# Optimization experiments

Hardware: AMD Instinct MI355X
Metric: run time of the kernel (lower is better)

The kernel has to match this reference:

```python
import jax, jax.numpy as jnp
import numpy as np

N_NODES = 100000
N_EDGES = 800000
D_IN = 128
D_H = 512


def _glorot(key, shape):
    fan_in, fan_out = shape[1], shape[0]
    lim = jnp.sqrt(6.0 / (fan_in + fan_out))
    return jax.random.uniform(key, shape, jnp.float32, -lim, lim)


def setup_inputs() -> dict:
    key = jax.random.key(0)
    ks = jax.random.split(key, 16)
    x = jax.random.normal(ks[0], (N_NODES, D_IN), jnp.float32)
    edge_index = jax.random.randint(ks[1], (2, N_EDGES), 0, N_NODES, jnp.int64)
    return {
        "x": x,
        "edge_index": edge_index,
        # SAGEConv layer1: lin_l (neighbors, with bias), lin_r (root, no bias)
        "Wl1": _glorot(ks[2], (D_H, D_IN)), "bl1": jnp.zeros((D_H,), jnp.float32),
        "Wr1": _glorot(ks[3], (D_H, D_IN)),
        # SAGEConv layer2
        "Wl2": _glorot(ks[4], (D_H, D_H)), "bl2": jnp.zeros((D_H,), jnp.float32),
        "Wr2": _glorot(ks[5], (D_H, D_H)),
        # SAGEConv layer3
        "Wl3": _glorot(ks[6], (D_H, D_H)), "bl3": jnp.zeros((D_H,), jnp.float32),
        "Wr3": _glorot(ks[7], (D_H, D_H)),
        # residual projections W, W2 (nn.Linear with bias)
        "Ww": _glorot(ks[8], (D_H, D_IN)), "bw": jnp.zeros((D_H,), jnp.float32),
        "Ww2": _glorot(ks[9], (D_H, D_IN)), "bw2": jnp.zeros((D_H,), jnp.float32),
        # shared PReLU parameter (nn.PReLU default: single param init 0.25)
        "a": jnp.array(0.25, jnp.float32),
    }


def _prelu(x, a):
    return jnp.where(x > 0, x, a * x)


def _sage_conv(x, src, dst, Wl, bl, Wr):
    # mean-aggregate neighbor features x[src] onto dst, then linear + root term
    msg = jax.ops.segment_sum(x[src], dst, num_segments=N_NODES)  # [N, d]
    deg = jax.ops.segment_sum(jnp.ones((src.shape[0],), x.dtype), dst,
                              num_segments=N_NODES)
    agg = msg / jnp.maximum(deg, 1.0)[:, None]
    return agg @ Wl.T + bl + x @ Wr.T


def reference(x, edge_index, Wl1, bl1, Wr1, Wl2, bl2, Wr2, Wl3, bl3, Wr3,
              Ww, bw, Ww2, bw2, a):
    src, dst = edge_index[0], edge_index[1]
    h1 = _prelu(_sage_conv(x, src, dst, Wl1, bl1, Wr1), a)
    h2 = _prelu(_sage_conv(h1 + (x @ Ww.T + bw), src, dst, Wl2, bl2, Wr2), a)
    h3 = _prelu(_sage_conv(h2 + h1 + (x @ Ww2.T + bw2), src, dst, Wl3, bl3, Wr3), a)
    return h3
```

## Files before the change

### kernel.cpp

```cpp
#include <hip/hip_runtime.h>
#include <stddef.h>

#define NN 100000
#define NE 800000
#define DIN 128
#define DH 512
#define MT 782
#define NWG1 (MT * 4)
#define CPX1 (NWG1 / 8)

typedef __attribute__((ext_vector_type(8))) short sh8;
typedef __attribute__((ext_vector_type(4))) float f32x4;

__device__ __forceinline__ unsigned short f2b(float f) {
  unsigned u = __float_as_uint(f);
  return (unsigned short)((u + 0x7FFFu + ((u >> 16) & 1u)) >> 16);
}
__device__ __forceinline__ float b2f(unsigned short s) {
  return __uint_as_float(((unsigned)s) << 16);
}

__device__ __forceinline__ void gload16(const unsigned short* g, unsigned short* l) {
  __builtin_amdgcn_global_load_lds(
      (const __attribute__((address_space(1))) void*)g,
      (__attribute__((address_space(3))) void*)l, 16, 0, 0);
}

#define SCHED_FENCE() __builtin_amdgcn_sched_barrier(0)
#define MEM_FENCE() asm volatile("" ::: "memory")
#define VMCNT(n) asm volatile("s_waitcnt vmcnt(" #n ")" ::: "memory")
#define LGKM0() asm volatile("s_waitcnt lgkmcnt(0)" ::: "memory")


__global__ void k_count(const int* __restrict__ dst, int* __restrict__ cnt) {
  int i = blockIdx.x * blockDim.x + threadIdx.x;
  if (i < NE) atomicAdd(&cnt[dst[i]], 1);
}

__global__ void k_invdeg(const int* __restrict__ cnt, float* __restrict__ inv_deg) {
  int i = blockIdx.x * blockDim.x + threadIdx.x;
  if (i < NN) inv_deg[i] = 1.0f / (float)(cnt[i] > 1 ? cnt[i] : 1);
}

__global__ void k_scan1(const int* __restrict__ cnt, int* __restrict__ excl,
                        int* __restrict__ partials) {
  __shared__ int sh[256];
  int tid = threadIdx.x;
  int base = blockIdx.x * 1024 + tid * 4;
  int v[4]; int s = 0;
#pragma unroll
  for (int i = 0; i < 4; i++) { int idx = base + i; v[i] = (idx < NN) ? cnt[idx] : 0; s += v[i]; }
  sh[tid] = s; __syncthreads();
  for (int off = 1; off < 256; off <<= 1) {
    int t = (tid >= off) ? sh[tid - off] : 0;
    __syncthreads();
    sh[tid] += t;
    __syncthreads();
  }
  int run = sh[tid] - s;
#pragma unroll
  for (int i = 0; i < 4; i++) { int idx = base + i; if (idx < NN) excl[idx] = run; run += v[i]; }
  if (tid == 255) partials[blockIdx.x] = sh[255];
}

__global__ void k_scan2(int* __restrict__ partials, int* __restrict__ row_start, int nparts) {
  __shared__ int sh[128];
  int tid = threadIdx.x;
  int v = (tid < nparts) ? partials[tid] : 0;
  sh[tid] = v; __syncthreads();
  for (int off = 1; off < 128; off <<= 1) {
    int t = (tid >= off) ? sh[tid - off] : 0;
    __syncthreads();
    sh[tid] += t;
    __syncthreads();
  }
  if (tid < nparts) partials[tid] = sh[tid] - v;
  if (tid == 127) row_start[NN] = sh[127];
}

__global__ void k_scan3(int* __restrict__ excl, const int* __restrict__ partials) {
  int i = blockIdx.x * blockDim.x + threadIdx.x;
  if (i < NN) excl[i] += partials[i >> 10];
}

__global__ void k_fill(const int* __restrict__ src, const int* __restrict__ dst,
                       const int* __restrict__ row_start, int* __restrict__ cursor,
                       int* __restrict__ ssrc) {
  int i = blockIdx.x * blockDim.x + threadIdx.x;
  if (i < NE) {
    int d = dst[i];
    int pos = atomicAdd(&cursor[d], 1);
    ssrc[row_start[d] + pos] = src[i];
  }
}


__global__ void k_f2b(const float* __restrict__ src, unsigned short* __restrict__ dst, int n) {
  int i = (blockIdx.x * blockDim.x + threadIdx.x) * 4;
  if (i < n) {
    float4 v = *(const float4*)(src + i);
    ushort4 o;
    o.x = f2b(v.x); o.y = f2b(v.y); o.z = f2b(v.z); o.w = f2b(v.w);
    *(ushort4*)(dst + i) = o;
  }
}


__global__ __launch_bounds__(256) void k_aggb512(
    const unsigned short* __restrict__ z, const int* __restrict__ rs,
    const int* __restrict__ ssrc, const float* __restrict__ inv_deg,
    unsigned short* __restrict__ agg) {
  int w = (blockIdx.x * blockDim.x + threadIdx.x) >> 6;
  int lane = threadIdx.x & 63;
  if (w >= NN) return;
  int e0 = rs[w], e1 = rs[w + 1];
  float acc[8] = {0, 0, 0, 0, 0, 0, 0, 0};
  int e = e0;
  for (; e + 1 < e1; e += 2) {
    int sa = ssrc[e], sb = ssrc[e + 1];
    sh8 va = *(const sh8*)(z + (size_t)sa * DH + lane * 8);
    sh8 vb = *(const sh8*)(z + (size_t)sb * DH + lane * 8);
#pragma unroll
    for (int j = 0; j < 8; ++j) acc[j] += b2f((unsigned short)va[j]) + b2f((unsigned short)vb[j]);
  }
  if (e < e1) {
    int sa = ssrc[e];
    sh8 va = *(const sh8*)(z + (size_t)sa * DH + lane * 8);
#pragma unroll
    for (int j = 0; j < 8; ++j) acc[j] += b2f((unsigned short)va[j]);
  }
  float s0 = inv_deg[w];
  sh8 o;
#pragma unroll
  for (int j = 0; j < 8; ++j) o[j] = (short)f2b(acc[j] * s0);
  *(sh8*)(agg + (size_t)w * DH + lane * 8) = o;
}

__global__ __launch_bounds__(256) void k_aggb128(
    const unsigned short* __restrict__ z, const int* __restrict__ rs,
    const int* __restrict__ ssrc, const float* __restrict__ inv_deg,
    unsigned short* __restrict__ agg) {
  int w = (blockIdx.x * blockDim.x + threadIdx.x) >> 6;
  int lane = threadIdx.x & 63;
  if (w >= NN) return;
  int e0 = rs[w], e1 = rs[w + 1];
  float a0 = 0.f, a1 = 0.f;
  int e = e0;
  for (; e + 1 < e1; e += 2) {
    int sa = ssrc[e], sb = ssrc[e + 1];
    unsigned va = *(const unsigned*)(z + (size_t)sa * DIN + lane * 2);
    unsigned vb = *(const unsigned*)(z + (size_t)sb * DIN + lane * 2);
    a0 += b2f((unsigned short)(va & 0xFFFFu)) + b2f((unsigned short)(vb & 0xFFFFu));
    a1 += b2f((unsigned short)(va >> 16)) + b2f((unsigned short)(vb >> 16));
  }
  if (e < e1) {
    unsigned va = *(const unsigned*)(z + (size_t)ssrc[e] * DIN + lane * 2);
    a0 += b2f((unsigned short)(va & 0xFFFFu));
    a1 += b2f((unsigned short)(va >> 16));
  }
  float s0 = inv_deg[w];
  unsigned o = (unsigned)f2b(a0 * s0) | ((unsigned)f2b(a1 * s0) << 16);
  *(unsigned*)(agg + (size_t)w * DIN + lane * 2) = o;
}


__device__ __forceinline__ void stage_tile(
    unsigned short* ldsA, unsigned short* ldsB,
    const unsigned short* __restrict__ A, int sA, int m0,
    const unsigned short* __restrict__ B, int sB, int n0,
    int k0, int tid) {
  const int w = tid >> 6, l = tid & 63;
  const int kc = (l & 3) * 8;
  const int rsub = l >> 2;
#pragma unroll
  for (int i = 0; i < 2; ++i) {
    int rl = w * 32 + i * 16 + rsub;
    int ra = m0 + rl; if (ra >= NN) ra = NN - 1;
    gload16(A + (size_t)ra * sA + k0 + kc, ldsA + (size_t)(w * 32 + i * 16) * 32);
    gload16(B + (size_t)(n0 + rl) * sB + k0 + kc, ldsB + (size_t)(w * 32 + i * 16) * 32);
  }
}

__device__ __forceinline__ void mfma_step(
    const unsigned short* As, const unsigned short* Bs,
    int wr, int wc, int r16, int kg, f32x4 (&acc)[4][4]) {
  sh8 af[4], bf[4];
#pragma unroll
  for (int i = 0; i < 4; ++i)
    af[i] = *(const sh8*)&As[(wr + i * 16 + r16) * 32 + kg * 8];
#pragma unroll
  for (int j = 0; j < 4; ++j)
    bf[j] = *(const sh8*)&Bs[(wc + j * 16 + r16) * 32 + kg * 8];
#pragma unroll
  for (int i = 0; i < 4; ++i)
#pragma unroll
    for (int j = 0; j < 4; ++j)
      acc[i][j] = __builtin_amdgcn_mfma_f32_16x16x32_bf16(af[i], bf[j], acc[i][j], 0, 0, 0);
}

#define PIPE_WAIT(s, S)                 \
  do {                                  \
    if ((s) < (S) - 2) VMCNT(8);        \
    else if ((s) == (S) - 2) VMCNT(4);  \
    else VMCNT(0);                      \
    SCHED_FENCE();                      \
    __builtin_amdgcn_s_barrier();       \
    MEM_FENCE(); SCHED_FENCE();         \
  } while (0)

#define PIPE_END()                      \
  do {                                  \
    SCHED_FENCE();                      \
    __builtin_amdgcn_s_barrier();       \
    MEM_FENCE(); SCHED_FENCE();         \
  } while (0)

__global__ __launch_bounds__(256, 2) void k_gemm1(
    const unsigned short* __restrict__ ag, const unsigned short* __restrict__ xb,
    const unsigned short* __restrict__ Wl1, const unsigned short* __restrict__ Wr1,
    const unsigned short* __restrict__ Ww, const unsigned short* __restrict__ Ww2,
    const float* __restrict__ bl1, const float* __restrict__ bw,
    const float* __restrict__ bw2, const float* __restrict__ aptr,
    unsigned short* __restrict__ z2o, unsigned short* __restrict__ z3po) {
  __shared__ __align__(16) unsigned short As[3][128 * 32];
  __shared__ __align__(16) unsigned short Bs[3][128 * 32];
  const int tid = threadIdx.x;
  const int b = blockIdx.x;
  const int L = (b & 7) * CPX1 + (b >> 3);
  const int m0 = (L >> 2) * 128, n0 = (L & 3) * 128;
  const int wid = tid >> 6, lane = tid & 63;
  const int r16 = lane & 15, kg = lane >> 4;
  const int wr = (wid >> 1) * 64, wc = (wid & 1) * 64;

  f32x4 a0[4][4], a1[4][4], a2[4][4];
#pragma unroll
  for (int i = 0; i < 4; ++i)
#pragma unroll
    for (int j = 0; j < 4; ++j) { a0[i][j] = 0.f; a1[i][j] = 0.f; a2[i][j] = 0.f; }

  auto stage = [&](int s, int buf) {
    const int seg = s >> 2, k0 = (s & 3) * 32;
    const unsigned short* Ap = (seg == 0) ? ag : xb;
    const unsigned short* Bp = (seg == 0) ? Wl1 : (seg == 1) ? Wr1 : (seg == 2) ? Ww : Ww2;
    stage_tile(As[buf], Bs[buf], Ap, DIN, m0, Bp, DIN, n0, k0, tid);
  };

  stage(0, 0);
  stage(1, 1);
  int cur = 0, nxt = 2;
  for (int s = 0; s < 16; ++s) {
    if (s + 2 < 16) stage(s + 2, nxt);
    PIPE_WAIT(s, 16);
    const int seg = s >> 2;
    __builtin_amdgcn_s_setprio(1);
    if (seg <= 1)      mfma_step(As[cur], Bs[cur], wr, wc, r16, kg, a0);
    else if (seg == 2) mfma_step(As[cur], Bs[cur], wr, wc, r16, kg, a1);
    else               mfma_step(As[cur], Bs[cur], wr, wc, r16, kg, a2);
    __builtin_amdgcn_s_setprio(0);
    PIPE_END();
    cur = (cur == 2) ? 0 : cur + 1;
    nxt = (nxt == 2) ? 0 : nxt + 1;
  }

  const float aval = aptr[0];
#pragma unroll
  for (int i = 0; i < 4; ++i) {
    const int mbase = m0 + wr + i * 16 + kg * 4;
#pragma unroll
    for (int j = 0; j < 4; ++j) {
      const int col = n0 + wc + j * 16 + r16;
      const float b1 = bl1[col], b2 = bw[col], b3 = bw2[col];
#pragma unroll
      for (int r = 0; r < 4; ++r) {
        const int m = mbase + r;
        if (m >= NN) continue;
        float h1 = a0[i][j][r] + b1;
        h1 = h1 > 0.f ? h1 : aval * h1;
        z2o[(size_t)m * DH + col] = f2b(h1 + a1[i][j][r] + b2);
        z3po[(size_t)m * DH + col] = f2b(h1 + a2[i][j][r] + b3);
      }
    }
  }
}


#define TILE_E 8192
#define NT23 32

__device__ __forceinline__ void stage_u(const unsigned short* __restrict__ src,
                                        int ld, int row0, int rowmax, int k0,
                                        unsigned short* lds, int u, int l) {
  int p = u * 8 + (l >> 3);
  int v = (l & 7) ^ (p & 7);
  int r = row0 + 2 * p + (v >> 2);
  if (r > rowmax) r = rowmax;
  gload16(src + (size_t)r * ld + k0 + (v & 3) * 8, lds + u * 512);
}

__device__ __forceinline__ sh8 frag(const unsigned short* lds, int r, int kg) {
  int p = r >> 1;
  int s = (((r & 1) << 2) | kg) ^ (p & 7);
  return *(const sh8*)(lds + p * 64 + s * 8);
}

template <bool LAST>
__global__ __launch_bounds__(512) void k8_gemm23(
    const unsigned short* __restrict__ Aag, const unsigned short* __restrict__ Az,
    const unsigned short* __restrict__ Wl, const unsigned short* __restrict__ Wr,
    const float* __restrict__ bl, const float* __restrict__ aptr,
    const unsigned short* __restrict__ z3p, void* __restrict__ outp) {
  __shared__ __align__(16) unsigned short LA[2][TILE_E];
  __shared__ __align__(16) unsigned short LB[2][TILE_E];
  const int b = blockIdx.x;
  const int xcd = b & 7, lo = b >> 3;
  const int wg = (xcd < 6 ? xcd * 98 : 588 + (xcd - 6) * 97) + lo;
  const int m0 = (wg >> 1) * 256, n0 = (wg & 1) * 256;
  const int tid = threadIdx.x, l = tid & 63, w = tid >> 6;
  const int r16 = l & 15, kg = l >> 4;
  const int rowA = (w >> 2) * 128, rowB = (w & 3) * 64;

  f32x4 acc[8][4];
#pragma unroll
  for (int i = 0; i < 8; ++i)
#pragma unroll
    for (int j = 0; j < 4; ++j) acc[i][j] = 0.f;

  auto stA = [&](int t) {
    const unsigned short* S = (t < 16) ? Aag : Az;
    const int k0 = (t & 15) * 32;
    unsigned short* d = LA[t & 1];
#pragma unroll
    for (int i = 0; i < 2; ++i) stage_u(S, DH, m0, NN - 1, k0, d, w * 2 + i, l);
  };
  auto stB = [&](int t) {
    const unsigned short* S = (t < 16) ? Wl : Wr;
    const int k0 = (t & 15) * 32;
    unsigned short* d = LB[t & 1];
#pragma unroll
    for (int i = 0; i < 2; ++i) stage_u(S, DH, n0, DH - 1, k0, d, w * 2 + i, l);
  };

  stA(0); stB(0);
  stA(1); stB(1);

  for (int t = 0; t < NT23; ++t) {
    if (t == NT23 - 1) { VMCNT(0); } else { VMCNT(4); }
    SCHED_FENCE();
    __builtin_amdgcn_s_barrier();
    MEM_FENCE(); SCHED_FENCE();
    const unsigned short* As = LA[t & 1];
    const unsigned short* Bs = LB[t & 1];
    sh8 bfr[4], afr[4];
#pragma unroll
    for (int j = 0; j < 4; ++j) bfr[j] = frag(Bs, rowB + j * 16 + r16, kg);
#pragma unroll
    for (int i = 0; i < 4; ++i) afr[i] = frag(As, rowA + i * 16 + r16, kg);
    __builtin_amdgcn_s_setprio(1);
#pragma unroll
    for (int i = 0; i < 4; ++i)
#pragma unroll
      for (int j = 0; j < 4; ++j)
        acc[i][j] = __builtin_amdgcn_mfma_f32_16x16x32_bf16(afr[i], bfr[j], acc[i][j], 0, 0, 0);
    __builtin_amdgcn_s_setprio(0);
#pragma unroll
    for (int i = 0; i < 4; ++i) afr[i] = frag(As, rowA + (i + 4) * 16 + r16, kg);
    LGKM0();
    SCHED_FENCE();
    __builtin_amdgcn_s_barrier();
    MEM_FENCE(); SCHED_FENCE();
    if (t + 2 < NT23) { stA(t + 2); stB(t + 2); }
    __builtin_amdgcn_s_setprio(1);
#pragma unroll
    for (int i = 0; i < 4; ++i)
#pragma unroll
      for (int j = 0; j < 4; ++j)
        acc[i + 4][j] = __builtin_amdgcn_mfma_f32_16x16x32_bf16(afr[i], bfr[j], acc[i + 4][j], 0, 0, 0);
    __builtin_amdgcn_s_setprio(0);
  }

  const float aval = aptr[0];
  float* outf = (float*)outp;
  unsigned short* outb = (unsigned short*)outp;
#pragma unroll
  for (int i = 0; i < 8; ++i) {
    const int mbase = m0 + rowA + i * 16 + kg * 4;
#pragma unroll
    for (int j = 0; j < 4; ++j) {
      const int col = n0 + rowB + j * 16 + r16;
      const float bv = bl[col];
#pragma unroll
      for (int r = 0; r < 4; ++r) {
        const int m = mbase + r;
        if (m >= NN) continue;
        float h = acc[i][j][r] + bv;
        h = h > 0.f ? h : aval * h;
        if constexpr (LAST) {
          outf[(size_t)m * DH + col] = h;
        } else {
          outb[(size_t)m * DH + col] = f2b(h + b2f(z3p[(size_t)m * DH + col]));
        }
      }
    }
  }
}


extern "C" void kernel_launch(void* const* d_in, const int* in_sizes, int n_in,
                              void* d_out, int out_size, void* d_ws, size_t ws_size,
                              hipStream_t stream) {
  const float* x = (const float*)d_in[0];
  const int* ei = (const int*)d_in[1];
  const float* Wl1 = (const float*)d_in[2];
  const float* bl1 = (const float*)d_in[3];
  const float* Wr1 = (const float*)d_in[4];
  const float* Wl2 = (const float*)d_in[5];
  const float* bl2 = (const float*)d_in[6];
  const float* Wr2 = (const float*)d_in[7];
  const float* Wl3 = (const float*)d_in[8];
  const float* bl3 = (const float*)d_in[9];
  const float* Wr3 = (const float*)d_in[10];
  const float* Ww  = (const float*)d_in[11];
  const float* bw  = (const float*)d_in[12];
  const float* Ww2 = (const float*)d_in[13];
  const float* bw2 = (const float*)d_in[14];
  const float* ap  = (const float*)d_in[15];
  float* out = (float*)d_out;

  const size_t MP = 100352;
  char* w = (char*)d_ws;
  size_t off = 0;
  unsigned short* xb   = (unsigned short*)(w + off); off += MP * DIN * 2;
  unsigned short* ag1  = (unsigned short*)(w + off); off += MP * DIN * 2;
  unsigned short* agb  = (unsigned short*)(w + off); off += MP * DH * 2;
  unsigned short* zb   = (unsigned short*)(w + off); off += MP * DH * 2;
  unsigned short* zc   = (unsigned short*)(w + off); off += MP * DH * 2;
  unsigned short* z3pb = (unsigned short*)(w + off); off += MP * DH * 2;
  unsigned short* Wl1b = (unsigned short*)(w + off); off += (size_t)DH * DIN * 2;
  unsigned short* Wr1b = (unsigned short*)(w + off); off += (size_t)DH * DIN * 2;
  unsigned short* Wwb  = (unsigned short*)(w + off); off += (size_t)DH * DIN * 2;
  unsigned short* Ww2b = (unsigned short*)(w + off); off += (size_t)DH * DIN * 2;
  unsigned short* Wl2b = (unsigned short*)(w + off); off += (size_t)DH * DH * 2;
  unsigned short* Wr2b = (unsigned short*)(w + off); off += (size_t)DH * DH * 2;
  unsigned short* Wl3b = (unsigned short*)(w + off); off += (size_t)DH * DH * 2;
  unsigned short* Wr3b = (unsigned short*)(w + off); off += (size_t)DH * DH * 2;
  float* inv_deg = (float*)(w + off); off += (size_t)NN * 4;
  int* row_start = (int*)(w + off); off += (size_t)(NN + 1) * 4;
  int* cursor = (int*)(w + off); off += (size_t)NN * 4;
  int* ssrc = (int*)(w + off); off += (size_t)NE * 4;
  int* partials = (int*)(w + off); off += 512;

  const int* esrc = ei;
  const int* edst = ei + NE;

  hipMemsetAsync(cursor, 0, NN * 4, stream);
  k_count<<<(NE + 255) / 256, 256, 0, stream>>>(edst, cursor);
  k_invdeg<<<(NN + 255) / 256, 256, 0, stream>>>(cursor, inv_deg);
  k_scan1<<<(NN + 1023) / 1024, 256, 0, stream>>>(cursor, row_start, partials);
  k_scan2<<<1, 128, 0, stream>>>(partials, row_start, (NN + 1023) / 1024);
  k_scan3<<<(NN + 255) / 256, 256, 0, stream>>>(row_start, partials);
  hipMemsetAsync(cursor, 0, NN * 4, stream);
  k_fill<<<(NE + 255) / 256, 256, 0, stream>>>(esrc, edst, row_start, cursor, ssrc);

  const int WK = DH * DIN;
  const int WB = DH * DH;
  k_f2b<<<(WK / 4 + 255) / 256, 256, 0, stream>>>(Wl1, Wl1b, WK);
  k_f2b<<<(WK / 4 + 255) / 256, 256, 0, stream>>>(Wr1, Wr1b, WK);
  k_f2b<<<(WK / 4 + 255) / 256, 256, 0, stream>>>(Ww,  Wwb,  WK);
  k_f2b<<<(WK / 4 + 255) / 256, 256, 0, stream>>>(Ww2, Ww2b, WK);
  k_f2b<<<(WB / 4 + 255) / 256, 256, 0, stream>>>(Wl2, Wl2b, WB);
  k_f2b<<<(WB / 4 + 255) / 256, 256, 0, stream>>>(Wr2, Wr2b, WB);
  k_f2b<<<(WB / 4 + 255) / 256, 256, 0, stream>>>(Wl3, Wl3b, WB);
  k_f2b<<<(WB / 4 + 255) / 256, 256, 0, stream>>>(Wr3, Wr3b, WB);
  k_f2b<<<(NN * DIN / 4 + 255) / 256, 256, 0, stream>>>(x, xb, NN * DIN);

  k_aggb128<<<(NN + 3) / 4, 256, 0, stream>>>(xb, row_start, ssrc, inv_deg, ag1);
  k_gemm1<<<NWG1, 256, 0, stream>>>(ag1, xb, Wl1b, Wr1b, Wwb, Ww2b, bl1, bw, bw2, ap,
                                    zb, z3pb);
  k_aggb512<<<(NN + 3) / 4, 256, 0, stream>>>(zb, row_start, ssrc, inv_deg, agb);
  k8_gemm23<false><<<782, 512, 0, stream>>>(agb, zb, Wl2b, Wr2b, bl2, ap, z3pb, zc);
  k_aggb512<<<(NN + 3) / 4, 256, 0, stream>>>(zc, row_start, ssrc, inv_deg, agb);
  k8_gemm23<true><<<782, 512, 0, stream>>>(agb, zc, Wl3b, Wr3b, bl3, ap, nullptr, out);
}
```

Baseline: 1.069 ms.

## Restructure layer 2/3 GEMM to keep weights in LDS and stream A directly

```diff
diff --git a/kernel.cpp b/kernel.cpp
--- a/kernel.cpp
+++ b/kernel.cpp
@@ -29,7 +29,6 @@
 #define SCHED_FENCE() __builtin_amdgcn_sched_barrier(0)
 #define MEM_FENCE() asm volatile("" ::: "memory")
 #define VMCNT(n) asm volatile("s_waitcnt vmcnt(" #n ")" ::: "memory")
-#define LGKM0() asm volatile("s_waitcnt lgkmcnt(0)" ::: "memory")
 
 
 __global__ void k_count(const int* __restrict__ dst, int* __restrict__ cnt) {
@@ -284,9 +283,6 @@
 }
 
 
-#define TILE_E 8192
-#define NT23 32
-
 __device__ __forceinline__ void stage_u(const unsigned short* __restrict__ src,
                                         int ld, int row0, int rowmax, int k0,
                                         unsigned short* lds, int u, int l) {
@@ -297,96 +293,97 @@
   gload16(src + (size_t)r * ld + k0 + (v & 3) * 8, lds + u * 512);
 }
 
-__device__ __forceinline__ sh8 frag(const unsigned short* lds, int r, int kg) {
-  int p = r >> 1;
-  int s = (((r & 1) << 2) | kg) ^ (p & 7);
-  return *(const sh8*)(lds + p * 64 + s * 8);
-}
-
 template <bool LAST>
-__global__ __launch_bounds__(512) void k8_gemm23(
+__global__ __launch_bounds__(512) void k_bl23(
     const unsigned short* __restrict__ Aag, const unsigned short* __restrict__ Az,
     const unsigned short* __restrict__ Wl, const unsigned short* __restrict__ Wr,
     const float* __restrict__ bl, const float* __restrict__ aptr,
     const unsigned short* __restrict__ z3p, void* __restrict__ outp) {
-  __shared__ __align__(16) unsigned short LA[2][TILE_E];
-  __shared__ __align__(16) unsigned short LB[2][TILE_E];
+  __shared__ __align__(16) unsigned short Bs[16 * 2048];
   const int b = blockIdx.x;
-  const int xcd = b & 7, lo = b >> 3;
-  const int wg = (xcd < 6 ? xcd * 98 : 588 + (xcd - 6) * 97) + lo;
-  const int m0 = (wg >> 1) * 256, n0 = (wg & 1) * 256;
+  const int nb = b & 7, mt = b >> 3;
+  const int n0 = nb * 64;
+  const int m0 = mt * 512;
   const int tid = threadIdx.x, l = tid & 63, w = tid >> 6;
   const int r16 = l & 15, kg = l >> 4;
-  const int rowA = (w >> 2) * 128, rowB = (w & 3) * 64;
-
-  f32x4 acc[8][4];
-#pragma unroll
-  for (int i = 0; i < 8; ++i)
+
+  int boff[4];
+#pragma unroll
+  for (int j = 0; j < 4; ++j) {
+    int r = j * 16 + r16;
+    int p = r >> 1;
+    int slot = (((r & 1) << 2) | kg) ^ (p & 7);
+    boff[j] = p * 64 + slot * 8;
+  }
+  int arow[4];
+#pragma unroll
+  for (int i = 0; i < 4; ++i) {
+    int r = m0 + w * 64 + i * 16 + r16;
+    arow[i] = r < NN ? r : NN - 1;
+  }
+
+  f32x4 acc[4][4];
+#pragma unroll
+  for (int i = 0; i < 4; ++i)
 #pragma unroll
     for (int j = 0; j < 4; ++j) acc[i][j] = 0.f;
 
-  auto stA = [&](int t) {
-    const unsigned short* S = (t < 16) ? Aag : Az;
-    const int k0 = (t & 15) * 32;
-    unsigned short* d = LA[t & 1];
-#pragma unroll
-    for (int i = 0; i < 2; ++i) stage_u(S, DH, m0, NN - 1, k0, d, w * 2 + i, l);
-  };
-  auto stB = [&](int t) {
-    const unsigned short* S = (t < 16) ? Wl : Wr;
-    const int k0 = (t & 15) * 32;
-    unsigned short* d = LB[t & 1];
-#pragma unroll
-    for (int i = 0; i < 2; ++i) stage_u(S, DH, n0, DH - 1, k0, d, w * 2 + i, l);
-  };
-
-  stA(0); stB(0);
-  stA(1); stB(1);
-
-  for (int t = 0; t < NT23; ++t) {
-    if (t == NT23 - 1) { VMCNT(0); } else { VMCNT(4); }
+#pragma unroll
+  for (int pass = 0; pass < 2; ++pass) {
+    const unsigned short* A = pass ? Az : Aag;
+    const unsigned short* W = pass ? Wr : Wl;
+    if (pass) {
+      SCHED_FENCE();
+      __builtin_amdgcn_s_barrier();
+      MEM_FENCE(); SCHED_FENCE();
+    }
+#pragma unroll
+    for (int q = 0; q < 8; ++q) {
+      int g = w * 8 + q;
+      int s = g >> 2, u = g & 3;
+      stage_u(W, DH, n0, DH - 1, s * 32, Bs + s * 2048, u, l);
+    }
+    VMCNT(0);
     SCHED_FENCE();
     __builtin_amdgcn_s_barrier();
     MEM_FENCE(); SCHED_FENCE();
-    const unsigned short* As = LA[t & 1];
-    const unsigned short* Bs = LB[t & 1];
-    sh8 bfr[4], afr[4];
-#pragma unroll
-    for (int j = 0; j < 4; ++j) bfr[j] = frag(Bs, rowB + j * 16 + r16, kg);
-#pragma unroll
-    for (int i = 0; i < 4; ++i) afr[i] = frag(As, rowA + i * 16 + r16, kg);
-    __builtin_amdgcn_s_setprio(1);
-#pragma unroll
-    for (int i = 0; i < 4; ++i)
-#pragma unroll
-      for (int j = 0; j < 4; ++j)
-        acc[i][j] = __builtin_amdgcn_mfma_f32_16x16x32_bf16(afr[i], bfr[j], acc[i][j], 0, 0, 0);
-    __builtin_amdgcn_s_setprio(0);
-#pragma unroll
-    for (int i = 0; i < 4; ++i) afr[i] = frag(As, rowA + (i + 4) * 16 + r16, kg);
-    LGKM0();
-    SCHED_FENCE();
-    __builtin_amdgcn_s_barrier();
-    MEM_FENCE(); SCHED_FENCE();
-    if (t + 2 < NT23) { stA(t + 2); stB(t + 2); }
-    __builtin_amdgcn_s_setprio(1);
-#pragma unroll
-    for (int i = 0; i < 4; ++i)
-#pragma unroll
-      for (int j = 0; j < 4; ++j)
-        acc[i + 4][j] = __builtin_amdgcn_mfma_f32_16x16x32_bf16(afr[i], bfr[j], acc[i + 4][j], 0, 0, 0);
-    __builtin_amdgcn_s_setprio(0);
+
+    const unsigned short* ap[4];
+#pragma unroll
+    for (int i = 0; i < 4; ++i) ap[i] = A + (size_t)arow[i] * DH + kg * 8;
+
+    sh8 ac[4];
+#pragma unroll
+    for (int i = 0; i < 4; ++i) ac[i] = *(const sh8*)ap[i];
+
+    for (int ks = 0; ks < 16; ++ks) {
+      sh8 an[4];
+      if (ks + 1 < 16) {
+#pragma unroll
+        for (int i = 0; i < 4; ++i) an[i] = *(const sh8*)(ap[i] + (ks + 1) * 32);
+      }
+      sh8 bf[4];
+#pragma unroll
+      for (int j = 0; j < 4; ++j) bf[j] = *(const sh8*)&Bs[ks * 2048 + boff[j]];
+#pragma unroll
+      for (int i = 0; i < 4; ++i)
+#pragma unroll
+        for (int j = 0; j < 4; ++j)
+          acc[i][j] = __builtin_amdgcn_mfma_f32_16x16x32_bf16(ac[i], bf[j], acc[i][j], 0, 0, 0);
+#pragma unroll
+      for (int i = 0; i < 4; ++i) ac[i] = an[i];
+    }
   }
 
   const float aval = aptr[0];
   float* outf = (float*)outp;
   unsigned short* outb = (unsigned short*)outp;
 #pragma unroll
-  for (int i = 0; i < 8; ++i) {
-    const int mbase = m0 + rowA + i * 16 + kg * 4;
+  for (int i = 0; i < 4; ++i) {
+    const int mbase = m0 + w * 64 + i * 16 + kg * 4;
 #pragma unroll
     for (int j = 0; j < 4; ++j) {
-      const int col = n0 + rowB + j * 16 + r16;
+      const int col = n0 + j * 16 + r16;
       const float bv = bl[col];
 #pragma unroll
       for (int r = 0; r < 4; ++r) {
@@ -477,7 +474,7 @@
   k_gemm1<<<NWG1, 256, 0, stream>>>(ag1, xb, Wl1b, Wr1b, Wwb, Ww2b, bl1, bw, bw2, ap,
                                     zb, z3pb);
   k_aggb512<<<(NN + 3) / 4, 256, 0, stream>>>(zb, row_start, ssrc, inv_deg, agb);
-  k8_gemm23<false><<<782, 512, 0, stream>>>(agb, zb, Wl2b, Wr2b, bl2, ap, z3pb, zc);
+  k_bl23<false><<<196 * 8, 512, 0, stream>>>(agb, zb, Wl2b, Wr2b, bl2, ap, z3pb, zc);
   k_aggb512<<<(NN + 3) / 4, 256, 0, stream>>>(zc, row_start, ssrc, inv_deg, agb);
-  k8_gemm23<true><<<782, 512, 0, stream>>>(agb, zc, Wl3b, Wr3b, bl3, ap, nullptr, out);
-}
+  k_bl23<true><<<196 * 8, 512, 0, stream>>>(agb, zc, Wl3b, Wr3b, bl3, ap, nullptr, out);
+}
```

After: 1.322 ms. 23.7% more time.

## Reshape layer-2/3 GEMM tiles to 128x512 full-width blocks with simpler pipeline

Applied to the files above, without the earlier changes.

```diff
diff --git a/kernel.cpp b/kernel.cpp
--- a/kernel.cpp
+++ b/kernel.cpp
@@ -29,7 +29,6 @@
 #define SCHED_FENCE() __builtin_amdgcn_sched_barrier(0)
 #define MEM_FENCE() asm volatile("" ::: "memory")
 #define VMCNT(n) asm volatile("s_waitcnt vmcnt(" #n ")" ::: "memory")
-#define LGKM0() asm volatile("s_waitcnt lgkmcnt(0)" ::: "memory")
 
 
 __global__ void k_count(const int* __restrict__ dst, int* __restrict__ cnt) {
@@ -284,9 +283,6 @@
 }
 
 
-#define TILE_E 8192
-#define NT23 32
-
 __device__ __forceinline__ void stage_u(const unsigned short* __restrict__ src,
                                         int ld, int row0, int rowmax, int k0,
                                         unsigned short* lds, int u, int l) {
@@ -304,77 +300,59 @@
 }
 
 template <bool LAST>
-__global__ __launch_bounds__(512) void k8_gemm23(
+__global__ __launch_bounds__(512) void k_wide23(
     const unsigned short* __restrict__ Aag, const unsigned short* __restrict__ Az,
     const unsigned short* __restrict__ Wl, const unsigned short* __restrict__ Wr,
     const float* __restrict__ bl, const float* __restrict__ aptr,
     const unsigned short* __restrict__ z3p, void* __restrict__ outp) {
-  __shared__ __align__(16) unsigned short LA[2][TILE_E];
-  __shared__ __align__(16) unsigned short LB[2][TILE_E];
-  const int b = blockIdx.x;
-  const int xcd = b & 7, lo = b >> 3;
-  const int wg = (xcd < 6 ? xcd * 98 : 588 + (xcd - 6) * 97) + lo;
-  const int m0 = (wg >> 1) * 256, n0 = (wg & 1) * 256;
+  __shared__ __align__(16) unsigned short LA[2][128 * 32];
+  __shared__ __align__(16) unsigned short LB[2][512 * 32];
+  const int m0 = blockIdx.x * 128;
   const int tid = threadIdx.x, l = tid & 63, w = tid >> 6;
   const int r16 = l & 15, kg = l >> 4;
-  const int rowA = (w >> 2) * 128, rowB = (w & 3) * 64;
-
-  f32x4 acc[8][4];
-#pragma unroll
-  for (int i = 0; i < 8; ++i)
-#pragma unroll
-    for (int j = 0; j < 4; ++j) acc[i][j] = 0.f;
-
-  auto stA = [&](int t) {
-    const unsigned short* S = (t < 16) ? Aag : Az;
+  const int wm = w >> 2, wn = w & 3;
+
+  f32x4 acc[4][8];
+#pragma unroll
+  for (int i = 0; i < 4; ++i)
+#pragma unroll
+    for (int j = 0; j < 8; ++j) acc[i][j] = 0.f;
+
+  auto stage = [&](int t) {
+    const unsigned short* A = (t < 16) ? Aag : Az;
+    const unsigned short* W = (t < 16) ? Wl : Wr;
     const int k0 = (t & 15) * 32;
-    unsigned short* d = LA[t & 1];
-#pragma unroll
-    for (int i = 0; i < 2; ++i) stage_u(S, DH, m0, NN - 1, k0, d, w * 2 + i, l);
+    unsigned short* la = LA[t & 1];
+    unsigned short* lb = LB[t & 1];
+    stage_u(A, DH, m0, NN - 1, k0, la, w, l);
+#pragma unroll
+    for (int q = 0; q < 4; ++q)
+      stage_u(W, DH, 0, DH - 1, k0, lb, w * 4 + q, l);
   };
-  auto stB = [&](int t) {
-    const unsigned short* S = (t < 16) ? Wl : Wr;
-    const int k0 = (t & 15) * 32;
-    unsigned short* d = LB[t & 1];
-#pragma unroll
-    for (int i = 0; i < 2; ++i) stage_u(S, DH, n0, DH - 1, k0, d, w * 2 + i, l);
-  };
-
-  stA(0); stB(0);
-  stA(1); stB(1);
-
-  for (int t = 0; t < NT23; ++t) {
-    if (t == NT23 - 1) { VMCNT(0); } else { VMCNT(4); }
+
+  stage(0);
+  for (int t = 0; t < 32; ++t) {
     SCHED_FENCE();
     __builtin_amdgcn_s_barrier();
     MEM_FENCE(); SCHED_FENCE();
-    const unsigned short* As = LA[t & 1];
-    const unsigned short* Bs = LB[t & 1];
-    sh8 bfr[4], afr[4];
-#pragma unroll
-    for (int j = 0; j < 4; ++j) bfr[j] = frag(Bs, rowB + j * 16 + r16, kg);
-#pragma unroll
-    for (int i = 0; i < 4; ++i) afr[i] = frag(As, rowA + i * 16 + r16, kg);
-    __builtin_amdgcn_s_setprio(1);
-#pragma unroll
-    for (int i = 0; i < 4; ++i)
-#pragma unroll
-      for (int j = 0; j < 4; ++j)
-        acc[i][j] = __builtin_amdgcn_mfma_f32_16x16x32_bf16(afr[i], bfr[j], acc[i][j], 0, 0, 0);
-    __builtin_amdgcn_s_setprio(0);
-#pragma unroll
-    for (int i = 0; i < 4; ++i) afr[i] = frag(As, rowA + (i + 4) * 16 + r16, kg);
-    LGKM0();
+    if (t + 1 < 32) { stage(t + 1); VMCNT(5); } else { VMCNT(0); }
     SCHED_FENCE();
     __builtin_amdgcn_s_barrier();
     MEM_FENCE(); SCHED_FENCE();
-    if (t + 2 < NT23) { stA(t + 2); stB(t + 2); }
+
+    const unsigned short* As = LA[t & 1];
+    const unsigned short* Bs = LB[t & 1];
+    sh8 afr[4], bfr[8];
+#pragma unroll
+    for (int i = 0; i < 4; ++i) afr[i] = frag(As, wm * 64 + i * 16 + r16, kg);
+#pragma unroll
+    for (int j = 0; j < 8; ++j) bfr[j] = frag(Bs, wn * 128 + j * 16 + r16, kg);
     __builtin_amdgcn_s_setprio(1);
 #pragma unroll
     for (int i = 0; i < 4; ++i)
 #pragma unroll
-      for (int j = 0; j < 4; ++j)
-        acc[i + 4][j] = __builtin_amdgcn_mfma_f32_16x16x32_bf16(afr[i], bfr[j], acc[i + 4][j], 0, 0, 0);
+      for (int j = 0; j < 8; ++j)
+        acc[i][j] = __builtin_amdgcn_mfma_f32_16x16x32_bf16(afr[i], bfr[j], acc[i][j], 0, 0, 0);
     __builtin_amdgcn_s_setprio(0);
   }
 
@@ -382,11 +360,11 @@
   float* outf = (float*)outp;
   unsigned short* outb = (unsigned short*)outp;
 #pragma unroll
-  for (int i = 0; i < 8; ++i) {
-    const int mbase = m0 + rowA + i * 16 + kg * 4;
-#pragma unroll
-    for (int j = 0; j < 4; ++j) {
-      const int col = n0 + rowB + j * 16 + r16;
+  for (int i = 0; i < 4; ++i) {
+    const int mbase = m0 + wm * 64 + i * 16 + kg * 4;
+#pragma unroll
+    for (int j = 0; j < 8; ++j) {
+      const int col = wn * 128 + j * 16 + r16;
       const float bv = bl[col];
 #pragma unroll
       for (int r = 0; r < 4; ++r) {
@@ -426,7 +404,7 @@
   const float* ap  = (const float*)d_in[15];
   float* out = (float*)d_out;
 
-  const size_t MP = 100352;
+  const size_t MP = 100096;
   char* w = (char*)d_ws;
   size_t off = 0;
   unsigned short* xb   = (unsigned short*)(w + off); off += MP * DIN * 2;
@@ -477,7 +455,7 @@
   k_gemm1<<<NWG1, 256, 0, stream>>>(ag1, xb, Wl1b, Wr1b, Wwb, Ww2b, bl1, bw, bw2, ap,
                                     zb, z3pb);
   k_aggb512<<<(NN + 3) / 4, 256, 0, stream>>>(zb, row_start, ssrc, inv_deg, agb);
-  k8_gemm23<false><<<782, 512, 0, stream>>>(agb, zb, Wl2b, Wr2b, bl2, ap, z3pb, zc);
+  k_wide23<false><<<MT, 512, 0, stream>>>(agb, zb, Wl2b, Wr2b, bl2, ap, z3pb, zc);
   k_aggb512<<<(NN + 3) / 4, 256, 0, stream>>>(zc, row_start, ssrc, inv_deg, agb);
-  k8_gemm23<true><<<782, 512, 0, stream>>>(agb, zc, Wl3b, Wr3b, bl3, ap, nullptr, out);
-}
+  k_wide23<true><<<MT, 512, 0, stream>>>(agb, zc, Wl3b, Wr3b, bl3, ap, nullptr, out);
+}
```

Measured after the change: 1.142 ms. 1.07x slower.
